# Kernel tuning notes

Measured on AMD Instinct MI355X. Metric: run time of the kernel, lower is better.

The kernel has to match this reference:

```python
import jax, jax.numpy as jnp
import numpy as np

H = 8        # heads
DK = 64      # dim_key
L = 64       # rel_pos_length
BN_EPS = 1e-5


def calc_reindexing_tensor(l, Lr):
    # Appendix B (5): band indicator of shape [l, l, 2L-1]
    x = jnp.arange(l)[:, None, None]
    i = jnp.arange(l)[None, :, None]
    r = jnp.arange(-(Lr - 1), Lr)[None, None, :]
    return ((i - x == r) & (jnp.abs(i - x) <= Lr)).astype(jnp.float32)


def setup_inputs() -> dict:
    key = jax.random.key(0)
    ks = jax.random.split(key, 6)
    b, c, x, y = 8, 256, 64, 64
    dim_hidden = H * DK
    return {
        "img": jax.random.normal(ks[0], (b, c, x, y), jnp.float32),
        "w_qkv": jax.random.normal(ks[1], (dim_hidden * 3, c), jnp.float32) * 0.02,
        "w_out": jax.random.normal(ks[2], (c, dim_hidden), jnp.float32) * 0.02,
        "b_out": jnp.zeros((c,), jnp.float32),
        "rel_rows": jax.random.normal(ks[3], (2 * L - 1, DK), jnp.float32),
        "rel_columns": jax.random.normal(ks[4], (2 * L - 1, DK), jnp.float32),
        "bn_gamma": jnp.ones((DK,), jnp.float32),
        "bn_beta": jnp.zeros((DK,), jnp.float32),
    }


def reference(img, w_qkv, w_out, b_out, rel_rows, rel_columns, bn_gamma, bn_beta):
    b, c, x, y = img.shape
    m = x * y
    # 1x1 conv (no bias) == channel GEMM
    qkv = jnp.einsum('bcxy,oc->boxy', img, w_qkv)
    q, k, v = jnp.split(qkv, 3, axis=1)
    # (b, H*DK, x, y) -> (b*H, DK, x*y)
    q = q.reshape(b * H, DK, m)
    k = k.reshape(b * H, DK, m)
    v = v.reshape(b * H, DK, m)

    # linear-attention content path
    k = jax.nn.softmax(k, axis=-1)
    context = jnp.einsum('ndm,nem->nde', k, v)          # (n, DK, DK)
    content_out = jnp.einsum('nde,ndm->nem', context, q)  # norm_queries=False
    content_out = content_out.reshape(b * H, DK, x, y)

    # relative-position path (dense banded einsums, faithful to original)
    q4 = q.reshape(b * H, DK, x, y)
    v4 = v.reshape(b * H, DK, x, y)
    Ix = calc_reindexing_tensor(x, L)                   # (x, x, 2L-1)
    Px = jnp.einsum('xir,rd->xid', Ix, rel_rows)        # (x, x, DK)
    Sx = jnp.einsum('ndxy,xid->nixy', q4, Px)
    Yh = jnp.einsum('nixy,neiy->nexy', Sx, v4)
    # BatchNorm2d(DK), training-mode batch stats over (n, x, y)
    mean = Yh.mean(axis=(0, 2, 3), keepdims=True)
    var = Yh.var(axis=(0, 2, 3), keepdims=True)
    Yh = (Yh - mean) * jax.lax.rsqrt(var + BN_EPS)
    Yh = Yh * bn_gamma[None, :, None, None] + bn_beta[None, :, None, None]

    Iy = Ix if x == y else calc_reindexing_tensor(y, L)
    Py = jnp.einsum('yir,rd->yid', Iy, rel_columns)     # (y, y, DK)
    Sy = jnp.einsum('ndxy,yid->nixy', q4, Py)
    rel_pos_out = jnp.einsum('nixy,nexi->nexy', Sy, Yh)

    out = content_out + rel_pos_out                     # (b*H, DK, x, y)
    out = out.reshape(b, H * DK, x, y)
    # 1x1 conv with bias
    return jnp.einsum('bcxy,oc->boxy', out, w_out) + b_out[None, :, None, None]
```

## Files before the change

kernel.cpp:

```cpp
#include <hip/hip_runtime.h>
#include <hip/hip_bf16.h>
#include <math.h>

#define NH   64
#define DKC  64
#define MM   4096
#define CC   256
#define RRN  127

typedef __hip_bfloat16 bf16;
__device__ __forceinline__ float b2f(bf16 x) { return __bfloat162float(x); }
__device__ __forceinline__ bf16 f2b(float x) { return __float2bfloat16(x); }
__device__ __forceinline__ unsigned short bbits(float x) { bf16 h = f2b(x); return *(unsigned short*)&h; }
__device__ __forceinline__ float fbits(unsigned short u) { bf16 h = *(bf16*)&u; return b2f(h); }

typedef short bf16x8 __attribute__((ext_vector_type(8)));
typedef float f32x4 __attribute__((ext_vector_type(4)));
typedef unsigned short u16;
typedef u16 u16x4 __attribute__((ext_vector_type(4)));

#define AS1 __attribute__((address_space(1)))
#define AS3 __attribute__((address_space(3)))
#define GLOAD16(gp, lp) __builtin_amdgcn_global_load_lds((const AS1 void*)(gp), (AS3 void*)(lp), 16, 0, 0)

__device__ __forceinline__ int swzsrc(int lane) { return 8 * ((lane & 7) ^ (lane >> 3)); }
#define FRSWZ(kelem, row) ((kelem) ^ (((row) & 7) * 8))

__global__ __launch_bounds__(256) void k_cvt_w(const float* __restrict__ w, bf16* __restrict__ wb) {
  const int i = blockIdx.x * 256 + threadIdx.x;
  wb[i] = f2b(w[i]);
}
__global__ __launch_bounds__(256) void k_cvt_w2(const float* __restrict__ w, bf16* __restrict__ wb) {
  const int i = blockIdx.x * 256 + threadIdx.x;
  wb[i] = f2b(w[i]);
}
__global__ __launch_bounds__(256) void k_cvt_rel(const float* __restrict__ r, bf16* __restrict__ rb) {
  const int i = blockIdx.x * 256 + threadIdx.x;
  rb[i] = (i < RRN * 64) ? f2b(r[i]) : f2b(0.f);
}
__global__ __launch_bounds__(256) void k_cvt_relr(const float* __restrict__ r, bf16* __restrict__ rb) {
  const int i = blockIdx.x * 256 + threadIdx.x;
  if (i < RRN * 64) rb[i] = f2b(r[i]);
}

__global__ __launch_bounds__(256) void k_timg(const float* __restrict__ img, bf16* __restrict__ imgT) {
  const int b = blockIdx.z, c0 = blockIdx.y * 64, m0 = blockIdx.x * 64;
  const int tid = threadIdx.x;
  __shared__ short T[64 * 66];
  const float* ib = img + ((size_t)b * CC + c0) * MM + m0;
#pragma unroll
  for (int j = 0; j < 4; ++j) {
    int f4 = j * 256 + tid;
    int cc = f4 >> 4, mm4 = (f4 & 15) * 4;
    f32x4 v = *(const f32x4*)&ib[(size_t)cc * MM + mm4];
#pragma unroll
    for (int k = 0; k < 4; ++k) T[cc * 66 + mm4 + k] = (short)bbits(v[k]);
  }
  __syncthreads();
  bf16* ob = imgT + ((size_t)b * MM + m0) * CC + c0;
#pragma unroll
  for (int j = 0; j < 4; ++j) {
    int f4 = j * 256 + tid;
    int mm = f4 >> 4, cc4 = (f4 & 15) * 4;
    u16x4 pk;
#pragma unroll
    for (int k = 0; k < 4; ++k) pk[k] = (u16)T[(cc4 + k) * 66 + mm];
    *(u16x4*)&ob[(size_t)mm * CC + cc4] = pk;
  }
}

__global__ __launch_bounds__(256) void k_qkv(const bf16* __restrict__ wb, const bf16* __restrict__ imgT,
                                             bf16* __restrict__ q, bf16* __restrict__ kk, bf16* __restrict__ v) {
  const int bI = blockIdx.z;
  const int o0 = blockIdx.y * 128;
  const int m0 = blockIdx.x * 128;
  const int tid = threadIdx.x;
  const int lane = tid & 63, wid = tid >> 6;
  const int fr = lane & 15;
  const int fq = lane >> 4;
  const int wm = (wid >> 1) * 64, wn = (wid & 1) * 64;

  __shared__ __align__(16) short As[128 * 64];
  __shared__ __align__(16) short Bs[128 * 64];

  const bf16* iB = imgT + (size_t)bI * MM * CC;

  f32x4 acc[4][4];
#pragma unroll
  for (int mi = 0; mi < 4; ++mi)
#pragma unroll
    for (int ni = 0; ni < 4; ++ni) acc[mi][ni] = (f32x4){0.f, 0.f, 0.f, 0.f};

  const int srow = lane >> 3;
  const int skc = swzsrc(lane);

  for (int kt = 0; kt < 4; ++kt) {
    const int k0 = kt * 64;
#pragma unroll
    for (int cc = 0; cc < 4; ++cc) {
      const int c = wid * 4 + cc;
      const int r = c * 8 + srow;
      GLOAD16(wb + (size_t)(o0 + r) * CC + k0 + skc, &As[c * 512]);
      GLOAD16(iB + (size_t)(m0 + r) * CC + k0 + skc, &Bs[c * 512]);
    }
    __syncthreads();
    bf16x8 af[4][2], bfr[4][2];
#pragma unroll
    for (int mi = 0; mi < 4; ++mi)
#pragma unroll
      for (int kkk = 0; kkk < 2; ++kkk)
        af[mi][kkk] = *(const bf16x8*)&As[(wm + mi * 16 + fr) * 64 + FRSWZ(kkk * 32 + fq * 8, fr)];
#pragma unroll
    for (int ni = 0; ni < 4; ++ni)
#pragma unroll
      for (int kkk = 0; kkk < 2; ++kkk)
        bfr[ni][kkk] = *(const bf16x8*)&Bs[(wn + ni * 16 + fr) * 64 + FRSWZ(kkk * 32 + fq * 8, fr)];
#pragma unroll
    for (int mi = 0; mi < 4; ++mi)
#pragma unroll
      for (int ni = 0; ni < 4; ++ni)
#pragma unroll
        for (int kkk = 0; kkk < 2; ++kkk)
          acc[mi][ni] = __builtin_amdgcn_mfma_f32_16x16x32_bf16(af[mi][kkk], bfr[ni][kkk], acc[mi][ni], 0, 0, 0);
    __syncthreads();
  }

#pragma unroll
  for (int mi = 0; mi < 4; ++mi) {
#pragma unroll
    for (int ni = 0; ni < 4; ++ni) {
      const int mcol = m0 + wn + ni * 16 + fr;
#pragma unroll
      for (int r = 0; r < 4; ++r) {
        int oo = o0 + wm + mi * 16 + fq * 4 + r;
        bf16* dst;
        if (oo < 512) { dst = q; }
        else if (oo < 1024) { dst = kk; oo -= 512; }
        else { dst = v; oo -= 1024; }
        dst[((size_t)bI * 512 + oo) * MM + mcol] = f2b(acc[mi][ni][r]);
      }
    }
  }
}

__global__ __launch_bounds__(256) void k_softmax(bf16* __restrict__ kk) {
  const size_t row = blockIdx.x;
  bf16* p = kk + row * (size_t)MM;
  const int t = threadIdx.x;
  __shared__ float sred[4];
  float v[16];
  float mx = -1e30f;
#pragma unroll
  for (int j = 0; j < 4; ++j) {
    u16x4 v4 = *(const u16x4*)&p[(j * 256 + t) * 4];
#pragma unroll
    for (int k = 0; k < 4; ++k) { v[j * 4 + k] = fbits(v4[k]); mx = fmaxf(mx, v[j * 4 + k]); }
  }
#pragma unroll
  for (int off = 32; off; off >>= 1) mx = fmaxf(mx, __shfl_down(mx, off));
  if ((t & 63) == 0) sred[t >> 6] = mx;
  __syncthreads();
  mx = fmaxf(fmaxf(sred[0], sred[1]), fmaxf(sred[2], sred[3]));
  __syncthreads();
  float s = 0.f;
#pragma unroll
  for (int i = 0; i < 16; ++i) { v[i] = expf(v[i] - mx); s += v[i]; }
#pragma unroll
  for (int off = 32; off; off >>= 1) s += __shfl_down(s, off);
  if ((t & 63) == 0) sred[t >> 6] = s;
  __syncthreads();
  s = sred[0] + sred[1] + sred[2] + sred[3];
  const float inv = 1.0f / s;
#pragma unroll
  for (int j = 0; j < 4; ++j) {
    u16x4 o;
#pragma unroll
    for (int k = 0; k < 4; ++k) o[k] = bbits(v[j * 4 + k] * inv);
    *(u16x4*)&p[(j * 256 + t) * 4] = o;
  }
}

__global__ __launch_bounds__(256) void k_ctx2(const bf16* __restrict__ kk, const bf16* __restrict__ v,
                                              float* __restrict__ part) {
  const int ch = blockIdx.x, n = blockIdx.y;
  const int tid = threadIdx.x;
  const int lane = tid & 63, wid = tid >> 6;
  const int fr = lane & 15, fq = lane >> 4;
  const int wr = (wid >> 1) * 32, wc = (wid & 1) * 32;
  __shared__ __align__(16) short Ks[64 * 64];
  __shared__ __align__(16) short Vs[64 * 64];
  const bf16* kp = kk + (size_t)n * DKC * MM;
  const bf16* vp = v + (size_t)n * DKC * MM;
  const int srow = lane >> 3;
  const int skc = swzsrc(lane);

  f32x4 acc[2][2];
#pragma unroll
  for (int mi = 0; mi < 2; ++mi)
#pragma unroll
    for (int ni = 0; ni < 2; ++ni) acc[mi][ni] = (f32x4){0.f, 0.f, 0.f, 0.f};

  for (int t = 0; t < 16; ++t) {
    const int m0 = ch * 1024 + t * 64;
#pragma unroll
    for (int cc = 0; cc < 4; ++cc) {
      const int c = wid * 4 + cc;
      if (c < 8) {
        const int r = c * 8 + srow;
        GLOAD16(kp + (size_t)r * MM + m0 + skc, &Ks[c * 512]);
      } else {
        const int r = (c - 8) * 8 + srow;
        GLOAD16(vp + (size_t)r * MM + m0 + skc, &Vs[(c - 8) * 512]);
      }
    }
    __syncthreads();
    bf16x8 af[2][2], bf[2][2];
#pragma unroll
    for (int mi = 0; mi < 2; ++mi)
#pragma unroll
      for (int kkx = 0; kkx < 2; ++kkx)
        af[mi][kkx] = *(const bf16x8*)&Ks[(wr + mi * 16 + fr) * 64 + FRSWZ(kkx * 32 + fq * 8, fr)];
#pragma unroll
    for (int ni = 0; ni < 2; ++ni)
#pragma unroll
      for (int kkx = 0; kkx < 2; ++kkx)
        bf[ni][kkx] = *(const bf16x8*)&Vs[(wc + ni * 16 + fr) * 64 + FRSWZ(kkx * 32 + fq * 8, fr)];
#pragma unroll
    for (int mi = 0; mi < 2; ++mi)
#pragma unroll
      for (int ni = 0; ni < 2; ++ni)
#pragma unroll
        for (int kkx = 0; kkx < 2; ++kkx)
          acc[mi][ni] = __builtin_amdgcn_mfma_f32_16x16x32_bf16(af[mi][kkx], bf[ni][kkx], acc[mi][ni], 0, 0, 0);
    __syncthreads();
  }
  float* pb = part + ((size_t)ch * NH + n) * 4096;
#pragma unroll
  for (int mi = 0; mi < 2; ++mi)
#pragma unroll
    for (int ni = 0; ni < 2; ++ni)
#pragma unroll
      for (int r = 0; r < 4; ++r)
        pb[(wr + mi * 16 + fq * 4 + r) * 64 + wc + ni * 16 + fr] = acc[mi][ni][r];
}

__global__ __launch_bounds__(256) void k_ctx_red(const float* __restrict__ part, float* __restrict__ ctx) {
  const int idx = blockIdx.x * 256 + threadIdx.x;
  float s = 0.f;
#pragma unroll
  for (int c = 0; c < 4; ++c) s += part[(size_t)c * 262144 + idx];
  ctx[idx] = s;
}

__global__ __launch_bounds__(256) void k_sx2(const bf16* __restrict__ relrb, const bf16* __restrict__ q,
                                             bf16* __restrict__ sxT) {
  const int x = blockIdx.x, n = blockIdx.y;
  const int tid = threadIdx.x;
  const int lane = tid & 63, wid = tid >> 6;
  const int fr = lane & 15, fq = lane >> 4;
  const int wr = (wid >> 1) * 32, wc = (wid & 1) * 32;
  __shared__ __align__(16) bf16 Qt[64 * 72];
  const size_t nb = (size_t)n * DKC * MM;
#pragma unroll
  for (int l = 0; l < 16; ++l) {
    int idx = tid + l * 256;
    int d = idx >> 6, y = idx & 63;
    Qt[y * 72 + (d ^ (8 * (y >> 3)))] = q[nb + (size_t)d * MM + x * 64 + y];
  }
  bf16x8 af[2][2];
#pragma unroll
  for (int mi = 0; mi < 2; ++mi) {
    const int j = wr + mi * 16 + fr + 63 - x;
#pragma unroll
    for (int kk = 0; kk < 2; ++kk)
      af[mi][kk] = *(const bf16x8*)&relrb[(size_t)j * 64 + kk * 32 + fq * 8];
  }
  __syncthreads();
  bf16x8 bq[2][2];
#pragma unroll
  for (int ni = 0; ni < 2; ++ni) {
    const int row = wc + ni * 16 + fr;
    const int swz = 8 * (row >> 3);
#pragma unroll
    for (int kk = 0; kk < 2; ++kk)
      bq[ni][kk] = *(const bf16x8*)&Qt[row * 72 + ((kk * 32 + fq * 8) ^ swz)];
  }
  f32x4 acc[2][2];
#pragma unroll
  for (int mi = 0; mi < 2; ++mi)
#pragma unroll
    for (int ni = 0; ni < 2; ++ni) acc[mi][ni] = (f32x4){0.f, 0.f, 0.f, 0.f};
#pragma unroll
  for (int mi = 0; mi < 2; ++mi)
#pragma unroll
    for (int ni = 0; ni < 2; ++ni)
#pragma unroll
      for (int kk = 0; kk < 2; ++kk)
        acc[mi][ni] = __builtin_amdgcn_mfma_f32_16x16x32_bf16(af[mi][kk], bq[ni][kk], acc[mi][ni], 0, 0, 0);
#pragma unroll
  for (int mi = 0; mi < 2; ++mi)
#pragma unroll
    for (int ni = 0; ni < 2; ++ni) {
      const int yy2 = wc + ni * 16 + fr;
      u16x4 pk;
#pragma unroll
      for (int r = 0; r < 4; ++r) pk[r] = bbits(acc[mi][ni][r]);
      *(u16x4*)&sxT[(((size_t)n * 64 + yy2) * 64 + x) * 64 + wr + mi * 16 + fq * 4] = pk;
    }
}

__global__ __launch_bounds__(256) void k_vt(const bf16* __restrict__ v, bf16* __restrict__ vT) {
  const int eg = blockIdx.x, n = blockIdx.y;
  const int tid = threadIdx.x;
  __shared__ short T[8 * 64 * 66];
  const bf16* vp = v + (size_t)n * DKC * MM + (size_t)eg * 8 * MM;
#pragma unroll
  for (int j = 0; j < 16; ++j) {
    int flat = (j * 256 + tid) * 8;
    int e = flat >> 12, m = flat & 4095;
    int x = m >> 6, y0 = m & 63;
    u16x4 lo = *(const u16x4*)&vp[(size_t)e * MM + m];
    u16x4 hi = *(const u16x4*)&vp[(size_t)e * MM + m + 4];
#pragma unroll
    for (int k = 0; k < 4; ++k) T[(e * 64 + y0 + k) * 66 + x] = (short)lo[k];
#pragma unroll
    for (int k = 0; k < 4; ++k) T[(e * 64 + y0 + 4 + k) * 66 + x] = (short)hi[k];
  }
  __syncthreads();
#pragma unroll
  for (int j = 0; j < 32; ++j) {
    int flat4 = j * 256 + tid;
    int x4 = flat4 & 15, e = (flat4 >> 4) & 7, y = flat4 >> 7;
    u16x4 pk;
#pragma unroll
    for (int r = 0; r < 4; ++r) pk[r] = (u16)T[(e * 64 + y) * 66 + x4 * 4 + r];
    *(u16x4*)&vT[(((size_t)n * 64 + y) * 64 + eg * 8 + e) * 64 + x4 * 4] = pk;
  }
}

__global__ __launch_bounds__(256) void k_yh2(const bf16* __restrict__ vT, const bf16* __restrict__ sxT,
                                             bf16* __restrict__ yhT) {
  const int y = blockIdx.x, n = blockIdx.y;
  const int tid = threadIdx.x;
  const int lane = tid & 63, wid = tid >> 6;
  const int fr = lane & 15, fq = lane >> 4;
  const int wr = (wid >> 1) * 32, wc = (wid & 1) * 32;
  __shared__ __align__(16) short Va[64 * 64];
  __shared__ __align__(16) short Sa[64 * 64];
  const size_t rb = ((size_t)n * 64 + y) * 4096;
  const int srow = lane >> 3;
  const int skc = swzsrc(lane);
#pragma unroll
  for (int cc = 0; cc < 2; ++cc) {
    const int c = wid * 2 + cc;
    const int r = c * 8 + srow;
    GLOAD16(vT + rb + (size_t)r * 64 + skc, &Va[c * 512]);
    GLOAD16(sxT + rb + (size_t)r * 64 + skc, &Sa[c * 512]);
  }
  __syncthreads();
  bf16x8 av[2][2], bs[2][2];
#pragma unroll
  for (int mi = 0; mi < 2; ++mi)
#pragma unroll
    for (int kk = 0; kk < 2; ++kk)
      av[mi][kk] = *(const bf16x8*)&Va[(wr + mi * 16 + fr) * 64 + FRSWZ(kk * 32 + fq * 8, fr)];
#pragma unroll
  for (int ni = 0; ni < 2; ++ni)
#pragma unroll
    for (int kk = 0; kk < 2; ++kk)
      bs[ni][kk] = *(const bf16x8*)&Sa[(wc + ni * 16 + fr) * 64 + FRSWZ(kk * 32 + fq * 8, fr)];
  f32x4 acc[2][2];
#pragma unroll
  for (int mi = 0; mi < 2; ++mi)
#pragma unroll
    for (int ni = 0; ni < 2; ++ni) acc[mi][ni] = (f32x4){0.f, 0.f, 0.f, 0.f};
#pragma unroll
  for (int mi = 0; mi < 2; ++mi)
#pragma unroll
    for (int ni = 0; ni < 2; ++ni)
#pragma unroll
      for (int kk = 0; kk < 2; ++kk)
        acc[mi][ni] = __builtin_amdgcn_mfma_f32_16x16x32_bf16(av[mi][kk], bs[ni][kk], acc[mi][ni], 0, 0, 0);
#pragma unroll
  for (int mi = 0; mi < 2; ++mi)
#pragma unroll
    for (int ni = 0; ni < 2; ++ni) {
      const int xo = wc + ni * 16 + fr;
      u16x4 pk;
#pragma unroll
      for (int r = 0; r < 4; ++r) pk[r] = bbits(acc[mi][ni][r]);
      *(u16x4*)&yhT[rb + (size_t)xo * 64 + wr + mi * 16 + fq * 4] = pk;
    }
}

__global__ __launch_bounds__(256) void k_bnpart2(const bf16* __restrict__ yhT, float* __restrict__ ps,
                                                 float* __restrict__ ps2) {
  const int gg = blockIdx.x, n = blockIdx.y;
  const int t = threadIdx.x;
  const int eq = (t & 15) * 4, rg = t >> 4;
  const bf16* p = yhT + (size_t)n * 262144 + (size_t)gg * 512 * 64;
  float s[4] = {}, s2[4] = {};
  for (int r = rg; r < 512; r += 16) {
    u16x4 v4 = *(const u16x4*)&p[(size_t)r * 64 + eq];
#pragma unroll
    for (int k = 0; k < 4; ++k) { float x = fbits(v4[k]); s[k] += x; s2[k] += x * x; }
  }
  __shared__ float ls[16][64], ls2[16][64];
#pragma unroll
  for (int k = 0; k < 4; ++k) { ls[rg][eq + k] = s[k]; ls2[rg][eq + k] = s2[k]; }
  __syncthreads();
  if (t < 64) {
    float S = 0.f, S2 = 0.f;
#pragma unroll
    for (int g = 0; g < 16; ++g) { S += ls[g][t]; S2 += ls2[g][t]; }
    ps[t * 512 + n * 8 + gg] = S;
    ps2[t * 512 + n * 8 + gg] = S2;
  }
}

__global__ __launch_bounds__(64) void k_bnfin(const float* __restrict__ ps, const float* __restrict__ ps2,
                                              float* __restrict__ mu, float* __restrict__ rs) {
  const int e = threadIdx.x;
  float S = 0.f, S2 = 0.f;
  for (int g = 0; g < 512; ++g) { S += ps[e * 512 + g]; S2 += ps2[e * 512 + g]; }
  const float invN = 1.0f / (NH * (float)MM);
  float m = S * invN;
  float var = S2 * invN - m * m;
  mu[e] = m;
  rs[e] = 1.0f / sqrtf(var + 1e-5f);
}

__global__ __launch_bounds__(256) void k_crc(const float* __restrict__ ctx, const bf16* __restrict__ q,
                                             const bf16* __restrict__ yhT, const bf16* __restrict__ relcb,
                                             const float* __restrict__ mu, const float* __restrict__ rs,
                                             const float* __restrict__ gamma, const float* __restrict__ beta,
                                             bf16* __restrict__ contentT) {
  const int xx = blockIdx.x, n = blockIdx.y;
  const int bI = n >> 3, h = n & 7;
  const int tid = threadIdx.x;
  const int lane = tid & 63, wv = tid >> 6;
  const int fr = lane & 15, fq = lane >> 4;
  __shared__ __align__(16) bf16 smem[4608 + 9216 + 4608 + 4608];
  bf16* Qt = smem;
  bf16* Scb = smem + 4608;
  bf16* Ysb = smem + 4608 + 9216;
  bf16* CT = smem + 4608 + 9216 + 4608;
  bf16* DT = smem;

  const size_t nb = (size_t)n * DKC * MM;
  const float* cn = ctx + (size_t)n * 4096;

#pragma unroll
  for (int l = 0; l < 16; ++l) {
    int idx = tid + l * 256;
    int d = idx >> 6, y = idx & 63;
    Qt[y * 72 + (d ^ (8 * (y >> 3)))] = q[nb + (size_t)d * MM + xx * 64 + y];
  }
#pragma unroll
  for (int l = 0; l < 16; ++l) {
    int idx = tid + l * 256;
    int i = idx >> 6, e = idx & 63;
    float val = (b2f(yhT[nb + (size_t)i * 4096 + xx * 64 + e]) - mu[e]) * rs[e] * gamma[e] + beta[e];
    Ysb[e * 72 + (i ^ (8 * (e >> 3)))] = f2b(val);
  }
#pragma unroll
  for (int l = 0; l < 16; ++l) {
    int idx = tid + l * 256;
    int d = idx >> 6, e = idx & 63;
    CT[e * 72 + (d ^ (8 * (e >> 3)))] = f2b(cn[idx]);
  }
  bf16x8 afr[2][2];
#pragma unroll
  for (int mi = 0; mi < 2; ++mi)
#pragma unroll
    for (int kk = 0; kk < 2; ++kk)
      afr[mi][kk] = *(const bf16x8*)&relcb[(size_t)(wv * 32 + mi * 16 + fr) * 64 + kk * 32 + fq * 8];
  __syncthreads();

  f32x4 acc1[2][4];
#pragma unroll
  for (int mi = 0; mi < 2; ++mi)
#pragma unroll
    for (int ni = 0; ni < 4; ++ni) acc1[mi][ni] = (f32x4){0.f, 0.f, 0.f, 0.f};
  bf16x8 bq[4][2];
#pragma unroll
  for (int ni = 0; ni < 4; ++ni) {
    const int row = ni * 16 + fr;
    const int swz = 8 * (row >> 3);
#pragma unroll
    for (int kk = 0; kk < 2; ++kk)
      bq[ni][kk] = *(const bf16x8*)&Qt[row * 72 + ((kk * 32 + fq * 8) ^ swz)];
  }
#pragma unroll
  for (int mi = 0; mi < 2; ++mi)
#pragma unroll
    for (int ni = 0; ni < 4; ++ni)
#pragma unroll
      for (int kk = 0; kk < 2; ++kk)
        acc1[mi][ni] = __builtin_amdgcn_mfma_f32_16x16x32_bf16(afr[mi][kk], bq[ni][kk], acc1[mi][ni], 0, 0, 0);
#pragma unroll
  for (int mi = 0; mi < 2; ++mi)
#pragma unroll
    for (int ni = 0; ni < 4; ++ni)
#pragma unroll
      for (int r = 0; r < 4; ++r)
        Scb[(wv * 32 + mi * 16 + fq * 4 + r) * 72 + ni * 16 + fr] = f2b(acc1[mi][ni][r]);
  bf16x8 aCT[2];
  {
    const int row = wv * 16 + fr;
    const int swz = 8 * (row >> 3);
#pragma unroll
    for (int kk = 0; kk < 2; ++kk)
      aCT[kk] = *(const bf16x8*)&CT[row * 72 + ((kk * 32 + fq * 8) ^ swz)];
  }
  __syncthreads();

#pragma unroll
  for (int l = 0; l < 16; ++l) {
    int idx = tid + l * 256;
    int y = idx >> 6, i = idx & 63;
    DT[y * 72 + i] = Scb[(i - y + 63) * 72 + y];
  }
  __syncthreads();

  f32x4 acc2[4];
#pragma unroll
  for (int ni = 0; ni < 4; ++ni) acc2[ni] = (f32x4){0.f, 0.f, 0.f, 0.f};
#pragma unroll
  for (int ni = 0; ni < 4; ++ni)
#pragma unroll
    for (int kk = 0; kk < 2; ++kk)
      acc2[ni] = __builtin_amdgcn_mfma_f32_16x16x32_bf16(aCT[kk], bq[ni][kk], acc2[ni], 0, 0, 0);
  bf16x8 a2[2], bd[4][2];
  {
    const int row = wv * 16 + fr;
    const int swz = 8 * (row >> 3);
#pragma unroll
    for (int kk = 0; kk < 2; ++kk)
      a2[kk] = *(const bf16x8*)&Ysb[row * 72 + ((kk * 32 + fq * 8) ^ swz)];
  }
#pragma unroll
  for (int ni = 0; ni < 4; ++ni)
#pragma unroll
    for (int kk = 0; kk < 2; ++kk)
      bd[ni][kk] = *(const bf16x8*)&DT[(ni * 16 + fr) * 72 + kk * 32 + fq * 8];
#pragma unroll
  for (int ni = 0; ni < 4; ++ni)
#pragma unroll
    for (int kk = 0; kk < 2; ++kk)
      acc2[ni] = __builtin_amdgcn_mfma_f32_16x16x32_bf16(a2[kk], bd[ni][kk], acc2[ni], 0, 0, 0);

  bf16* cb = contentT + (size_t)bI * MM * 512;
#pragma unroll
  for (int ni = 0; ni < 4; ++ni) {
    size_t a = (size_t)(xx * 64 + ni * 16 + fr) * 512 + h * 64 + wv * 16 + fq * 4;
    u16x4 pk;
#pragma unroll
    for (int r = 0; r < 4; ++r) pk[r] = bbits(acc2[ni][r]);
    *(u16x4*)&cb[a] = pk;
  }
}

__global__ __launch_bounds__(256) void k_final(const bf16* __restrict__ wb2, const bf16* __restrict__ cT,
                                               const float* __restrict__ bout, float* __restrict__ dout) {
  const int bI = blockIdx.z;
  const int o0 = blockIdx.y * 128;
  const int m0 = blockIdx.x * 128;
  const int tid = threadIdx.x;
  const int lane = tid & 63, wid = tid >> 6;
  const int fr = lane & 15;
  const int fq = lane >> 4;
  const int wm = (wid >> 1) * 64, wn = (wid & 1) * 64;

  __shared__ __align__(16) short As[128 * 64];
  __shared__ __align__(16) short Bs[128 * 64];

  const bf16* cB = cT + (size_t)bI * MM * 512;

  f32x4 acc[4][4];
#pragma unroll
  for (int mi = 0; mi < 4; ++mi)
#pragma unroll
    for (int ni = 0; ni < 4; ++ni) acc[mi][ni] = (f32x4){0.f, 0.f, 0.f, 0.f};

  const int srow = lane >> 3;
  const int skc = swzsrc(lane);

  for (int kt = 0; kt < 8; ++kt) {
    const int k0 = kt * 64;
#pragma unroll
    for (int cc = 0; cc < 4; ++cc) {
      const int c = wid * 4 + cc;
      const int r = c * 8 + srow;
      GLOAD16(wb2 + (size_t)(o0 + r) * 512 + k0 + skc, &As[c * 512]);
      GLOAD16(cB + (size_t)(m0 + r) * 512 + k0 + skc, &Bs[c * 512]);
    }
    __syncthreads();
    bf16x8 af[4][2], bfr[4][2];
#pragma unroll
    for (int mi = 0; mi < 4; ++mi)
#pragma unroll
      for (int kkk = 0; kkk < 2; ++kkk)
        af[mi][kkk] = *(const bf16x8*)&As[(wm + mi * 16 + fr) * 64 + FRSWZ(kkk * 32 + fq * 8, fr)];
#pragma unroll
    for (int ni = 0; ni < 4; ++ni)
#pragma unroll
      for (int kkk = 0; kkk < 2; ++kkk)
        bfr[ni][kkk] = *(const bf16x8*)&Bs[(wn + ni * 16 + fr) * 64 + FRSWZ(kkk * 32 + fq * 8, fr)];
#pragma unroll
    for (int mi = 0; mi < 4; ++mi)
#pragma unroll
      for (int ni = 0; ni < 4; ++ni)
#pragma unroll
        for (int kkk = 0; kkk < 2; ++kkk)
          acc[mi][ni] = __builtin_amdgcn_mfma_f32_16x16x32_bf16(af[mi][kkk], bfr[ni][kkk], acc[mi][ni], 0, 0, 0);
    __syncthreads();
  }

#pragma unroll
  for (int mi = 0; mi < 4; ++mi) {
#pragma unroll
    for (int ni = 0; ni < 4; ++ni) {
      const int mcol = m0 + wn + ni * 16 + fr;
#pragma unroll
      for (int r = 0; r < 4; ++r) {
        const int oo = o0 + wm + mi * 16 + fq * 4 + r;
        dout[((size_t)bI * 256 + oo) * MM + mcol] = acc[mi][ni][r] + bout[oo];
      }
    }
  }
}

extern "C" void kernel_launch(void* const* d_in, const int* in_sizes, int n_in,
                              void* d_out, int out_size, void* d_ws, size_t ws_size,
                              hipStream_t stream) {
  const float* img = (const float*)d_in[0];
  const float* w_qkv = (const float*)d_in[1];
  const float* w_out = (const float*)d_in[2];
  const float* b_out = (const float*)d_in[3];
  const float* rel_rows = (const float*)d_in[4];
  const float* rel_cols = (const float*)d_in[5];
  const float* gamma = (const float*)d_in[6];
  const float* beta = (const float*)d_in[7];
  float* out = (float*)d_out;

  const size_t SZ = (size_t)NH * DKC * MM;
  bf16* q = (bf16*)d_ws;
  bf16* kbuf = q + SZ;
  bf16* vbuf = kbuf + SZ;
  bf16* imgT = vbuf + SZ;
  float* ctxp = (float*)imgT;
  float* ctx = ctxp + 4 * 262144;
  float* ps = ctx + 262144;
  float* ps2 = ps + 32768;
  float* mu = ps2 + 32768;
  float* rs = mu + 64;
  bf16* wb = imgT + 8388608;
  bf16* sxbuf = wb + 393216;
  bf16* wb2 = sxbuf + SZ;
  bf16* relcb = wb2 + 131072;
  bf16* relrb = relcb + 8192;

  k_cvt_w<<<1536, 256, 0, stream>>>(w_qkv, wb);
  k_cvt_w2<<<512, 256, 0, stream>>>(w_out, wb2);
  k_cvt_rel<<<32, 256, 0, stream>>>(rel_cols, relcb);
  k_cvt_relr<<<32, 256, 0, stream>>>(rel_rows, relrb);
  k_timg<<<dim3(64, 4, 8), 256, 0, stream>>>(img, imgT);
  k_qkv<<<dim3(32, 12, 8), 256, 0, stream>>>(wb, imgT, q, kbuf, vbuf);
  k_softmax<<<4096, 256, 0, stream>>>(kbuf);
  k_ctx2<<<dim3(4, 64), 256, 0, stream>>>(kbuf, vbuf, ctxp);
  k_ctx_red<<<1024, 256, 0, stream>>>(ctxp, ctx);
  k_sx2<<<dim3(64, 64), 256, 0, stream>>>(relrb, q, sxbuf);
  k_vt<<<dim3(8, 64), 256, 0, stream>>>(vbuf, kbuf);
  k_yh2<<<dim3(64, 64), 256, 0, stream>>>(kbuf, sxbuf, vbuf);
  k_bnpart2<<<dim3(8, 64), 256, 0, stream>>>(vbuf, ps, ps2);
  k_bnfin<<<1, 64, 0, stream>>>(ps, ps2, mu, rs);
  k_crc<<<dim3(64, 64), 256, 0, stream>>>(ctx, q, vbuf, relcb, mu, rs, gamma, beta, sxbuf);
  k_final<<<dim3(32, 2, 8), 256, 0, stream>>>(wb2, sxbuf, b_out, out);
}
```

Measured before the change: 221.6 us.

## Store Q transposed from QKV GEMM and load it via direct global-to-LDS copies

The QKV GEMM epilogue now writes Q in a position-major, head-dim-contiguous layout with packed 4-element stores. k_sx2 and k_crc then fill their Q tiles with 16-byte global_load_lds copies into a swizzled LDS layout, replacing strided per-element gathers and transposes. The four weight-conversion kernels are also merged into a single launch. The Q epilogue store pattern changes and depends on the swizzle matching in both consumers.

```diff
diff --git a/kernel.cpp b/kernel.cpp
--- a/kernel.cpp
+++ b/kernel.cpp
@@ -26,21 +26,20 @@
 __device__ __forceinline__ int swzsrc(int lane) { return 8 * ((lane & 7) ^ (lane >> 3)); }
 #define FRSWZ(kelem, row) ((kelem) ^ (((row) & 7) * 8))
 
-__global__ __launch_bounds__(256) void k_cvt_w(const float* __restrict__ w, bf16* __restrict__ wb) {
+__global__ __launch_bounds__(256) void k_cvt_all(const float* __restrict__ w_qkv, const float* __restrict__ w_out,
+                                                 const float* __restrict__ relc, const float* __restrict__ relr,
+                                                 bf16* __restrict__ wb, bf16* __restrict__ wb2,
+                                                 bf16* __restrict__ relcb, bf16* __restrict__ relrb) {
   const int i = blockIdx.x * 256 + threadIdx.x;
-  wb[i] = f2b(w[i]);
-}
-__global__ __launch_bounds__(256) void k_cvt_w2(const float* __restrict__ w, bf16* __restrict__ wb) {
-  const int i = blockIdx.x * 256 + threadIdx.x;
-  wb[i] = f2b(w[i]);
-}
-__global__ __launch_bounds__(256) void k_cvt_rel(const float* __restrict__ r, bf16* __restrict__ rb) {
-  const int i = blockIdx.x * 256 + threadIdx.x;
-  rb[i] = (i < RRN * 64) ? f2b(r[i]) : f2b(0.f);
-}
-__global__ __launch_bounds__(256) void k_cvt_relr(const float* __restrict__ r, bf16* __restrict__ rb) {
-  const int i = blockIdx.x * 256 + threadIdx.x;
-  if (i < RRN * 64) rb[i] = f2b(r[i]);
+  if (i < 393216) {
+    wb[i] = f2b(w_qkv[i]);
+  } else if (i < 524288) {
+    int j = i - 393216; wb2[j] = f2b(w_out[j]);
+  } else if (i < 532480) {
+    int j = i - 524288; relcb[j] = (j < RRN * 64) ? f2b(relc[j]) : f2b(0.f);
+  } else {
+    int j = i - 532480; if (j < RRN * 64) relrb[j] = f2b(relr[j]);
+  }
 }
 
 __global__ __launch_bounds__(256) void k_timg(const float* __restrict__ img, bf16* __restrict__ imgT) {
@@ -70,7 +69,7 @@
 }
 
 __global__ __launch_bounds__(256) void k_qkv(const bf16* __restrict__ wb, const bf16* __restrict__ imgT,
-                                             bf16* __restrict__ q, bf16* __restrict__ kk, bf16* __restrict__ v) {
+                                             bf16* __restrict__ qT, bf16* __restrict__ kk, bf16* __restrict__ v) {
   const int bI = blockIdx.z;
   const int o0 = blockIdx.y * 128;
   const int m0 = blockIdx.x * 128;
@@ -125,19 +124,34 @@
     __syncthreads();
   }
 
-#pragma unroll
-  for (int mi = 0; mi < 4; ++mi) {
-#pragma unroll
-    for (int ni = 0; ni < 4; ++ni) {
-      const int mcol = m0 + wn + ni * 16 + fr;
-#pragma unroll
-      for (int r = 0; r < 4; ++r) {
-        int oo = o0 + wm + mi * 16 + fq * 4 + r;
-        bf16* dst;
-        if (oo < 512) { dst = q; }
-        else if (oo < 1024) { dst = kk; oo -= 512; }
-        else { dst = v; oo -= 1024; }
-        dst[((size_t)bI * 512 + oo) * MM + mcol] = f2b(acc[mi][ni][r]);
+  if (o0 < 512) {
+    const int nglob = bI * 8 + ((o0 + wm) >> 6);
+#pragma unroll
+    for (int mi = 0; mi < 4; ++mi) {
+      const int d0 = mi * 16 + fq * 4;
+#pragma unroll
+      for (int ni = 0; ni < 4; ++ni) {
+        const int mcol = m0 + wn + ni * 16 + fr;
+        u16x4 pk;
+#pragma unroll
+        for (int r = 0; r < 4; ++r) pk[r] = bbits(acc[mi][ni][r]);
+        *(u16x4*)&qT[((size_t)nglob * MM + mcol) * 64 + d0] = pk;
+      }
+    }
+  } else {
+#pragma unroll
+    for (int mi = 0; mi < 4; ++mi) {
+#pragma unroll
+      for (int ni = 0; ni < 4; ++ni) {
+        const int mcol = m0 + wn + ni * 16 + fr;
+#pragma unroll
+        for (int r = 0; r < 4; ++r) {
+          int oo = o0 + wm + mi * 16 + fq * 4 + r;
+          bf16* dst;
+          if (oo < 1024) { dst = kk; oo -= 512; }
+          else { dst = v; oo -= 1024; }
+          dst[((size_t)bI * 512 + oo) * MM + mcol] = f2b(acc[mi][ni][r]);
+        }
       }
     }
   }
@@ -252,20 +266,21 @@
   ctx[idx] = s;
 }
 
-__global__ __launch_bounds__(256) void k_sx2(const bf16* __restrict__ relrb, const bf16* __restrict__ q,
+__global__ __launch_bounds__(256) void k_sx2(const bf16* __restrict__ relrb, const bf16* __restrict__ qT,
                                              bf16* __restrict__ sxT) {
   const int x = blockIdx.x, n = blockIdx.y;
   const int tid = threadIdx.x;
   const int lane = tid & 63, wid = tid >> 6;
   const int fr = lane & 15, fq = lane >> 4;
   const int wr = (wid >> 1) * 32, wc = (wid & 1) * 32;
-  __shared__ __align__(16) bf16 Qt[64 * 72];
-  const size_t nb = (size_t)n * DKC * MM;
-#pragma unroll
-  for (int l = 0; l < 16; ++l) {
-    int idx = tid + l * 256;
-    int d = idx >> 6, y = idx & 63;
-    Qt[y * 72 + (d ^ (8 * (y >> 3)))] = q[nb + (size_t)d * MM + x * 64 + y];
+  __shared__ __align__(16) short Qt[64 * 64];
+  const bf16* qrow = qT + ((size_t)n * MM + x * 64) * 64;
+  const int srow = lane >> 3, skc = swzsrc(lane);
+#pragma unroll
+  for (int cc = 0; cc < 2; ++cc) {
+    const int c = wid * 2 + cc;
+    const int r = c * 8 + srow;
+    GLOAD16(qrow + (size_t)r * 64 + skc, &Qt[c * 512]);
   }
   bf16x8 af[2][2];
 #pragma unroll
@@ -280,10 +295,9 @@
 #pragma unroll
   for (int ni = 0; ni < 2; ++ni) {
     const int row = wc + ni * 16 + fr;
-    const int swz = 8 * (row >> 3);
-#pragma unroll
-    for (int kk = 0; kk < 2; ++kk)
-      bq[ni][kk] = *(const bf16x8*)&Qt[row * 72 + ((kk * 32 + fq * 8) ^ swz)];
+#pragma unroll
+    for (int kk = 0; kk < 2; ++kk)
+      bq[ni][kk] = *(const bf16x8*)&Qt[row * 64 + FRSWZ(kk * 32 + fq * 8, fr)];
   }
   f32x4 acc[2][2];
 #pragma unroll
@@ -430,7 +444,7 @@
   rs[e] = 1.0f / sqrtf(var + 1e-5f);
 }
 
-__global__ __launch_bounds__(256) void k_crc(const float* __restrict__ ctx, const bf16* __restrict__ q,
+__global__ __launch_bounds__(256) void k_crc(const float* __restrict__ ctx, const bf16* __restrict__ qT,
                                              const bf16* __restrict__ yhT, const bf16* __restrict__ relcb,
                                              const float* __restrict__ mu, const float* __restrict__ rs,
                                              const float* __restrict__ gamma, const float* __restrict__ beta,
@@ -440,21 +454,25 @@
   const int tid = threadIdx.x;
   const int lane = tid & 63, wv = tid >> 6;
   const int fr = lane & 15, fq = lane >> 4;
-  __shared__ __align__(16) bf16 smem[4608 + 9216 + 4608 + 4608];
-  bf16* Qt = smem;
-  bf16* Scb = smem + 4608;
-  bf16* Ysb = smem + 4608 + 9216;
-  bf16* CT = smem + 4608 + 9216 + 4608;
-  bf16* DT = smem;
+  __shared__ __align__(16) short smem[4096 + 9216 + 4608 + 4608];
+  short* Qt = smem;
+  bf16* Scb = (bf16*)(smem + 4096);
+  bf16* Ysb = (bf16*)(smem + 4096 + 9216);
+  bf16* CT = (bf16*)(smem + 4096 + 9216 + 4608);
+  short* DT = smem;
 
   const size_t nb = (size_t)n * DKC * MM;
   const float* cn = ctx + (size_t)n * 4096;
 
-#pragma unroll
-  for (int l = 0; l < 16; ++l) {
-    int idx = tid + l * 256;
-    int d = idx >> 6, y = idx & 63;
-    Qt[y * 72 + (d ^ (8 * (y >> 3)))] = q[nb + (size_t)d * MM + xx * 64 + y];
+  {
+    const bf16* qrow = qT + ((size_t)n * MM + xx * 64) * 64;
+    const int srow = lane >> 3, skc = swzsrc(lane);
+#pragma unroll
+    for (int cc = 0; cc < 2; ++cc) {
+      const int c = wv * 2 + cc;
+      const int r = c * 8 + srow;
+      GLOAD16(qrow + (size_t)r * 64 + skc, &Qt[c * 512]);
+    }
   }
 #pragma unroll
   for (int l = 0; l < 16; ++l) {
@@ -486,10 +504,9 @@
 #pragma unroll
   for (int ni = 0; ni < 4; ++ni) {
     const int row = ni * 16 + fr;
-    const int swz = 8 * (row >> 3);
-#pragma unroll
-    for (int kk = 0; kk < 2; ++kk)
-      bq[ni][kk] = *(const bf16x8*)&Qt[row * 72 + ((kk * 32 + fq * 8) ^ swz)];
+#pragma unroll
+    for (int kk = 0; kk < 2; ++kk)
+      bq[ni][kk] = *(const bf16x8*)&Qt[row * 64 + FRSWZ(kk * 32 + fq * 8, fr)];
   }
 #pragma unroll
   for (int mi = 0; mi < 2; ++mi)
@@ -519,7 +536,7 @@
   for (int l = 0; l < 16; ++l) {
     int idx = tid + l * 256;
     int y = idx >> 6, i = idx & 63;
-    DT[y * 72 + i] = Scb[(i - y + 63) * 72 + y];
+    DT[y * 64 + FRSWZ(i, y)] = *(const short*)&Scb[(i - y + 63) * 72 + y];
   }
   __syncthreads();
 
@@ -540,10 +557,12 @@
       a2[kk] = *(const bf16x8*)&Ysb[row * 72 + ((kk * 32 + fq * 8) ^ swz)];
   }
 #pragma unroll
-  for (int ni = 0; ni < 4; ++ni)
-#pragma unroll
-    for (int kk = 0; kk < 2; ++kk)
-      bd[ni][kk] = *(const bf16x8*)&DT[(ni * 16 + fr) * 72 + kk * 32 + fq * 8];
+  for (int ni = 0; ni < 4; ++ni) {
+    const int row = ni * 16 + fr;
+#pragma unroll
+    for (int kk = 0; kk < 2; ++kk)
+      bd[ni][kk] = *(const bf16x8*)&DT[row * 64 + FRSWZ(kk * 32 + fq * 8, fr)];
+  }
 #pragma unroll
   for (int ni = 0; ni < 4; ++ni)
 #pragma unroll
@@ -645,8 +664,8 @@
   float* out = (float*)d_out;
 
   const size_t SZ = (size_t)NH * DKC * MM;
-  bf16* q = (bf16*)d_ws;
-  bf16* kbuf = q + SZ;
+  bf16* qbuf = (bf16*)d_ws;
+  bf16* kbuf = qbuf + SZ;
   bf16* vbuf = kbuf + SZ;
   bf16* imgT = vbuf + SZ;
   float* ctxp = (float*)imgT;
@@ -661,20 +680,17 @@
   bf16* relcb = wb2 + 131072;
   bf16* relrb = relcb + 8192;
 
-  k_cvt_w<<<1536, 256, 0, stream>>>(w_qkv, wb);
-  k_cvt_w2<<<512, 256, 0, stream>>>(w_out, wb2);
-  k_cvt_rel<<<32, 256, 0, stream>>>(rel_cols, relcb);
-  k_cvt_relr<<<32, 256, 0, stream>>>(rel_rows, relrb);
+  k_cvt_all<<<2112, 256, 0, stream>>>(w_qkv, w_out, rel_cols, rel_rows, wb, wb2, relcb, relrb);
   k_timg<<<dim3(64, 4, 8), 256, 0, stream>>>(img, imgT);
-  k_qkv<<<dim3(32, 12, 8), 256, 0, stream>>>(wb, imgT, q, kbuf, vbuf);
+  k_qkv<<<dim3(32, 12, 8), 256, 0, stream>>>(wb, imgT, qbuf, kbuf, vbuf);
   k_softmax<<<4096, 256, 0, stream>>>(kbuf);
   k_ctx2<<<dim3(4, 64), 256, 0, stream>>>(kbuf, vbuf, ctxp);
   k_ctx_red<<<1024, 256, 0, stream>>>(ctxp, ctx);
-  k_sx2<<<dim3(64, 64), 256, 0, stream>>>(relrb, q, sxbuf);
+  k_sx2<<<dim3(64, 64), 256, 0, stream>>>(relrb, qbuf, sxbuf);
   k_vt<<<dim3(8, 64), 256, 0, stream>>>(vbuf, kbuf);
   k_yh2<<<dim3(64, 64), 256, 0, stream>>>(kbuf, sxbuf, vbuf);
   k_bnpart2<<<dim3(8, 64), 256, 0, stream>>>(vbuf, ps, ps2);
   k_bnfin<<<1, 64, 0, stream>>>(ps, ps2, mu, rs);
-  k_crc<<<dim3(64, 64), 256, 0, stream>>>(ctx, q, vbuf, relcb, mu, rs, gamma, beta, sxbuf);
+  k_crc<<<dim3(64, 64), 256, 0, stream>>>(ctx, qbuf, vbuf, relcb, mu, rs, gamma, beta, sxbuf);
   k_final<<<dim3(32, 2, 8), 256, 0, stream>>>(wb2, sxbuf, b_out, out);
 }
```

Result: faster. 207.6 us (-6.3%).
